# Kernel tuning notes

Hardware: AMD Instinct MI355X
Metric: run time of the kernel (lower is better)

## Reference

```python
import jax, jax.numpy as jnp
import numpy as np

N_NODES = 100000
N_EDGES = 1600000
N_IN = 512
N_H = 64


def setup_inputs() -> dict:
    key = jax.random.key(0)
    ks = jax.random.split(key, 9)
    x_1 = jax.random.normal(ks[0], (1, N_NODES, N_IN), dtype=jnp.float32)
    x_2 = jax.random.normal(ks[1], (1, N_NODES, N_IN), dtype=jnp.float32)
    edge_row = jax.random.randint(ks[2], (N_EDGES,), 0, N_NODES, dtype=jnp.int32)
    edge_col = jax.random.randint(ks[3], (N_EDGES,), 0, N_NODES, dtype=jnp.int32)
    edge_weight = jax.random.uniform(ks[4], (N_EDGES,), dtype=jnp.float32)
    # GCN fc: Linear(n_in, n_h, bias=False), xavier_uniform init
    lim_fc = float(np.sqrt(6.0 / (N_IN + N_H)))
    fc_weight = jax.random.uniform(ks[5], (N_H, N_IN), minval=-lim_fc, maxval=lim_fc, dtype=jnp.float32)
    gcn_bias = jnp.zeros((N_H,), dtype=jnp.float32)
    prelu_a = jnp.array(0.25, dtype=jnp.float32)  # nn.PReLU default single weight
    lim_lin = float(np.sqrt(1.0 / N_H))  # torch Linear default init bound
    lin_weight = jax.random.uniform(ks[6], (N_H, N_H), minval=-lim_lin, maxval=lim_lin, dtype=jnp.float32)
    lin_bias = jax.random.uniform(ks[7], (N_H,), minval=-lim_lin, maxval=lim_lin, dtype=jnp.float32)
    return {
        "x_1": x_1, "x_2": x_2,
        "edge_row": edge_row, "edge_col": edge_col, "edge_weight": edge_weight,
        "fc_weight": fc_weight, "gcn_bias": gcn_bias, "prelu_a": prelu_a,
        "lin_weight": lin_weight, "lin_bias": lin_bias,
    }


def reference(x_1, x_2, edge_row, edge_col, edge_weight,
              fc_weight, gcn_bias, prelu_a, lin_weight, lin_bias):
    def gcn(x):
        # fc: [1,N,F] @ W^T -> [N, H]
        h = jnp.einsum('bnf,hf->bnh', x, fc_weight)[0]
        # spmm: out[r] += w * h[c]  (COO adjacency)
        msgs = edge_weight[:, None] * h[edge_col]            # [E, H]
        agg = jax.ops.segment_sum(msgs, edge_row, num_segments=N_NODES)
        out = agg + gcn_bias
        return jnp.where(out >= 0, out, prelu_a * out)       # PReLU, shape [N, H]

    h_1 = gcn(x_1)
    h_2 = gcn(x_2)
    z_1 = (h_1 @ lin_weight.T + lin_bias).sum(axis=1)        # [N]
    z_2 = (h_2 @ lin_weight.T + lin_bias).sum(axis=1)        # [N]
    return jnp.concatenate([z_1, z_2], axis=0)               # [2N]
```

## Files before the change

kernel.cpp:

```cpp
#include <hip/hip_runtime.h>

#define F_IN 512
#define HDIM 64
#define RSHIFT 7
#define RWIDTH 128
#define MAXNB 1024
#define CHUNK 4096
#define BK 32

typedef _Float16 f16;
typedef _Float16 f16x2 __attribute__((ext_vector_type(2)));
typedef _Float16 f16x8 __attribute__((ext_vector_type(8)));
typedef float f32x4 __attribute__((ext_vector_type(4)));

#define GLOAD_LDS16(src, dst)                                                        \
    __builtin_amdgcn_global_load_lds((const __attribute__((address_space(1))) void*)(src), \
                                     (__attribute__((address_space(3))) void*)(dst), 16, 0, 0)

__global__ void prep_kernel(const float* __restrict__ linW,
                            const float* __restrict__ linB,
                            float* __restrict__ wsum) {
    int k = threadIdx.x;
    float s = 0.f;
    for (int j = 0; j < HDIM; ++j) s += linW[j * HDIM + k];
    wsum[k] = s;
    if (k == 0) {
        float b = 0.f;
        for (int j = 0; j < HDIM; ++j) b += linB[j];
        wsum[HDIM] = b;
    }
}

__global__ __launch_bounds__(256) void prep_w16_kernel(const float* __restrict__ W,
                                                       f16* __restrict__ wf) {
    int t = blockIdx.x * 256 + threadIdx.x;
    int s = t >> 8;
    int c = (t >> 6) & 3;
    int l = t & 63;
    int row = c * 16 + (l & 15);
    int kb = s * 32 + ((l >> 4) << 3);
#pragma unroll
    for (int j = 0; j < 8; ++j)
        wf[(size_t)t * 8 + j] = (f16)W[row * F_IN + kb + j];
}

__global__ void zero_int_kernel(int* __restrict__ p, int n) {
    int i = blockIdx.x * blockDim.x + threadIdx.x;
    if (i < n) p[i] = 0;
}

__global__ __launch_bounds__(256) void bhist_kernel(const int* __restrict__ row,
                                                    int* __restrict__ bh,
                                                    int n_edges, int NB) {
    __shared__ int lh[MAXNB];
    for (int i = threadIdx.x; i < NB; i += 256) lh[i] = 0;
    __syncthreads();
    for (int e = blockIdx.x * 256 + threadIdx.x; e < n_edges; e += gridDim.x * 256)
        atomicAdd(&lh[row[e] >> RSHIFT], 1);
    __syncthreads();
    for (int i = threadIdx.x; i < NB; i += 256)
        if (lh[i]) atomicAdd(&bh[i], lh[i]);
}

__global__ __launch_bounds__(1024) void bscan_kernel(const int* __restrict__ bh,
                                                     int* __restrict__ boff,
                                                     int* __restrict__ gcur,
                                                     int* __restrict__ ptr,
                                                     int NB, int n_nodes, int n_edges) {
    __shared__ int s[1024];
    const int t = threadIdx.x;
    int v = (t < NB) ? bh[t] : 0;
    s[t] = v;
    __syncthreads();
#pragma unroll
    for (int off = 1; off < 1024; off <<= 1) {
        int x = (t >= off) ? s[t - off] : 0;
        __syncthreads();
        s[t] += x;
        __syncthreads();
    }
    if (t < NB) {
        int o = s[t] - v;
        boff[t] = o;
        gcur[t] = o;
    }
    if (t == NB) boff[NB] = n_edges;
    if (t == 0) ptr[n_nodes] = n_edges;
}

__global__ __launch_bounds__(256) void part_kernel(const int* __restrict__ row,
                                                   const int* __restrict__ col,
                                                   const float* __restrict__ w,
                                                   int* __restrict__ gcur,
                                                   int2* __restrict__ etmp,
                                                   int n_edges, int NB) {
    __shared__ int2 stg[CHUNK];
    __shared__ unsigned short sbin[CHUNK];
    __shared__ int lh[MAXNB];
    __shared__ int lofs[MAXNB];
    __shared__ int psum[256];
    const int t = threadIdx.x;
    const int base = blockIdx.x * CHUNK;
    const int cnt = min(CHUNK, n_edges - base);

    for (int i = t; i < NB; i += 256) lh[i] = 0;
    __syncthreads();
    for (int i = t; i < cnt; i += 256)
        atomicAdd(&lh[row[base + i] >> RSHIFT], 1);
    __syncthreads();
    int loc[4];
    int s0 = 0;
#pragma unroll
    for (int j = 0; j < 4; ++j) {
        int b = t * 4 + j;
        int c = (b < NB) ? lh[b] : 0;
        loc[j] = s0;
        s0 += c;
    }
    psum[t] = s0;
    __syncthreads();
#pragma unroll
    for (int off = 1; off < 256; off <<= 1) {
        int x = (t >= off) ? psum[t - off] : 0;
        __syncthreads();
        psum[t] += x;
        __syncthreads();
    }
    int pbase = psum[t] - s0;
#pragma unroll
    for (int j = 0; j < 4; ++j) {
        int b = t * 4 + j;
        if (b < NB) lofs[b] = pbase + loc[j];
    }
    __syncthreads();
    for (int i = t; i < cnt; i += 256) {
        int r = row[base + i];
        int b = r >> RSHIFT;
        int p = atomicAdd(&lofs[b], 1);
        stg[p] = make_int2(__float_as_int(w[base + i]),
                           (col[base + i] << RSHIFT) | (r & (RWIDTH - 1)));
        sbin[p] = (unsigned short)b;
    }
    __syncthreads();
    for (int b = t; b < NB; b += 256) {
        int c = lh[b];
        if (c) {
            int lstart = lofs[b] - c;
            int gb = atomicAdd(&gcur[b], c);
            lh[b] = gb - lstart;
        }
    }
    __syncthreads();
    for (int p = t; p < cnt; p += 256) {
        int b = sbin[p];
        etmp[lh[b] + p] = stg[p];
    }
}

__global__ __launch_bounds__(256) void bsort_kernel(const int* __restrict__ boff,
                                                    const int2* __restrict__ etmp,
                                                    int2* __restrict__ ebin,
                                                    int* __restrict__ ptr,
                                                    int n_nodes) {
    __shared__ int nh[RWIDTH], lo[RWIDTH], lc[RWIDTH];
    const int b = blockIdx.x;
    const int t = threadIdx.x;
    const int e0 = boff[b], e1 = boff[b + 1];
    const int cnt = e1 - e0;
    if (t < RWIDTH) nh[t] = 0;
    __syncthreads();
    for (int i = t; i < cnt; i += 256)
        atomicAdd(&nh[etmp[e0 + i].y & (RWIDTH - 1)], 1);
    __syncthreads();
    if (t < RWIDTH) lo[t] = nh[t];
    __syncthreads();
    for (int off = 1; off < RWIDTH; off <<= 1) {
        int x = 0;
        if (t < RWIDTH && t >= off) x = lo[t - off];
        __syncthreads();
        if (t < RWIDTH) lo[t] += x;
        __syncthreads();
    }
    if (t < RWIDTH) {
        int ex = lo[t] - nh[t];
        lc[t] = ex;
        int node = b * RWIDTH + t;
        if (node < n_nodes) ptr[node] = e0 + ex;
    }
    __syncthreads();
    for (int i = t; i < cnt; i += 256) {
        int2 r = etmp[e0 + i];
        int p = atomicAdd(&lc[r.y & (RWIDTH - 1)], 1);
        ebin[e0 + p] = make_int2(r.x, r.y >> RSHIFT);
    }
}

__global__ __launch_bounds__(256, 4) void gemm_both_kernel(const float* __restrict__ X1,
                                                           const float* __restrict__ X2,
                                                           const f16* __restrict__ wf,
                                                           f16* __restrict__ H,
                                                           int n_nodes) {
    __shared__ float4 xs_v[2048];
    char* xs = (char*)xs_v;
    const int t = threadIdx.x;
    const int l = t & 63;
    const int w = t >> 6;
    const int m0 = blockIdx.x * 64;
    const f16x8* wfv = reinterpret_cast<const f16x8*>(wf);

    const int srow_off = l >> 3;
    const int sswz = (((l & 7) ^ (l >> 3)) << 4);

#define STAGE(c, buf)                                                                   \
    {                                                                                   \
        _Pragma("unroll")                                                               \
        for (int p = 0; p < 4; ++p) {                                                   \
            int row = ((p & 1) << 5) + (w << 3) + srow_off;                             \
            int gm = m0 + row;                                                          \
            if (gm >= n_nodes) gm = n_nodes - 1;                                        \
            const float* Xp = (p >> 1) ? X2 : X1;                                       \
            const char* src = (const char*)(Xp + (size_t)gm * F_IN + (c) * BK) + sswz;  \
            GLOAD_LDS16(src, xs + (buf) * 16384 + p * 4096 + w * 1024);                 \
        }                                                                               \
    }

    const int rl = w * 16 + (l & 15);
    const int g = l >> 4;
    const int swz = (rl & 7) << 4;

    f32x4 a00 = {}, a01 = {}, a02 = {}, a03 = {};
    f32x4 a10 = {}, a11 = {}, a12 = {}, a13 = {};

    STAGE(0, 0)
    __syncthreads();
    int buf = 0;
#pragma unroll 2
    for (int c = 0; c < 16; ++c) {
        if (c < 15) STAGE(c + 1, buf ^ 1)
        const f16x8* bp = wfv + (size_t)(c * 4) * 64 + l;
        f16x8 b0 = bp[0];
        f16x8 b1 = bp[64];
        f16x8 b2 = bp[128];
        f16x8 b3 = bp[192];
        const char* base = xs + buf * 16384 + rl * 128;
#pragma unroll
        for (int pass = 0; pass < 2; ++pass) {
            float4 xa = *reinterpret_cast<const float4*>(base + pass * 8192 + ((g * 32) ^ swz));
            float4 xb = *reinterpret_cast<const float4*>(base + pass * 8192 + ((g * 32 + 16) ^ swz));
            f16x8 a;
            a[0] = (f16)xa.x; a[1] = (f16)xa.y; a[2] = (f16)xa.z; a[3] = (f16)xa.w;
            a[4] = (f16)xb.x; a[5] = (f16)xb.y; a[6] = (f16)xb.z; a[7] = (f16)xb.w;
            if (pass == 0) {
                a00 = __builtin_amdgcn_mfma_f32_16x16x32_f16(a, b0, a00, 0, 0, 0);
                a01 = __builtin_amdgcn_mfma_f32_16x16x32_f16(a, b1, a01, 0, 0, 0);
                a02 = __builtin_amdgcn_mfma_f32_16x16x32_f16(a, b2, a02, 0, 0, 0);
                a03 = __builtin_amdgcn_mfma_f32_16x16x32_f16(a, b3, a03, 0, 0, 0);
            } else {
                a10 = __builtin_amdgcn_mfma_f32_16x16x32_f16(a, b0, a10, 0, 0, 0);
                a11 = __builtin_amdgcn_mfma_f32_16x16x32_f16(a, b1, a11, 0, 0, 0);
                a12 = __builtin_amdgcn_mfma_f32_16x16x32_f16(a, b2, a12, 0, 0, 0);
                a13 = __builtin_amdgcn_mfma_f32_16x16x32_f16(a, b3, a13, 0, 0, 0);
            }
        }
        __syncthreads();
        buf ^= 1;
    }
#undef STAGE

    {
        f16* tile = (f16*)xs;
        const int colj = l & 15;
        const int rbase = w * 16 + g * 4;
#pragma unroll
        for (int j = 0; j < 4; ++j) {
            f16* tp = tile + (rbase + j) * 128 + colj * 2;
            tp[0]  = (f16)a00[j];
            tp[1]  = (f16)a10[j];
            tp[32] = (f16)a01[j];
            tp[33] = (f16)a11[j];
            tp[64] = (f16)a02[j];
            tp[65] = (f16)a12[j];
            tp[96] = (f16)a03[j];
            tp[97] = (f16)a13[j];
        }
        __syncthreads();
        const int row = t >> 2;
        const int gm = m0 + row;
        if (gm < n_nodes) {
            const float4* sp = reinterpret_cast<const float4*>(xs + row * 256 + (t & 3) * 64);
            float4* dp = reinterpret_cast<float4*>((char*)H + (size_t)gm * 256 + (t & 3) * 64);
#pragma unroll
            for (int q = 0; q < 4; ++q) dp[q] = sp[q];
        }
    }
}

__global__ __launch_bounds__(256) void agg_both_kernel(const int* __restrict__ ptr,
                                                       const int2* __restrict__ ebin,
                                                       const f16* __restrict__ h,
                                                       const float* __restrict__ gbias,
                                                       const float* __restrict__ wsum,
                                                       const float* __restrict__ prelu_a,
                                                       float* __restrict__ z,
                                                       int n_nodes) {
    const int lane = threadIdx.x & 63;
    const int wv = threadIdx.x >> 6;
    const int n = blockIdx.x * 4 + wv;
    if (n >= n_nodes) return;
    const f16x2* hv = reinterpret_cast<const f16x2*>(h) + lane;
    const int p0 = __builtin_amdgcn_readfirstlane(ptr[n]);
    const int p1 = __builtin_amdgcn_readfirstlane(ptr[n + 1]);
    float acc1 = 0.f, acc2 = 0.f;
    int i = p0;
    for (; i + 3 < p1; i += 4) {
        int2 e0 = ebin[i];
        int2 e1 = ebin[i + 1];
        int2 e2 = ebin[i + 2];
        int2 e3 = ebin[i + 3];
        f16x2 h0 = hv[(size_t)e0.y * HDIM];
        f16x2 h1 = hv[(size_t)e1.y * HDIM];
        f16x2 h2 = hv[(size_t)e2.y * HDIM];
        f16x2 h3 = hv[(size_t)e3.y * HDIM];
        float w0 = __int_as_float(e0.x), w1 = __int_as_float(e1.x);
        float w2 = __int_as_float(e2.x), w3 = __int_as_float(e3.x);
        acc1 = fmaf(w0, (float)h0[0], acc1);
        acc2 = fmaf(w0, (float)h0[1], acc2);
        acc1 = fmaf(w1, (float)h1[0], acc1);
        acc2 = fmaf(w1, (float)h1[1], acc2);
        acc1 = fmaf(w2, (float)h2[0], acc1);
        acc2 = fmaf(w2, (float)h2[1], acc2);
        acc1 = fmaf(w3, (float)h3[0], acc1);
        acc2 = fmaf(w3, (float)h3[1], acc2);
    }
    for (; i < p1; ++i) {
        int2 e0 = ebin[i];
        f16x2 h0 = hv[(size_t)e0.y * HDIM];
        float w0 = __int_as_float(e0.x);
        acc1 = fmaf(w0, (float)h0[0], acc1);
        acc2 = fmaf(w0, (float)h0[1], acc2);
    }
    const float a = prelu_a[0];
    const float gb = gbias[lane];
    const float wl = wsum[lane];
    float v1 = acc1 + gb;
    float v2 = acc2 + gb;
    v1 = (v1 >= 0.f) ? v1 : a * v1;
    v2 = (v2 >= 0.f) ? v2 : a * v2;
    float q1 = v1 * wl;
    float q2 = v2 * wl;
#pragma unroll
    for (int m = 32; m >= 1; m >>= 1) {
        q1 += __shfl_xor(q1, m, 64);
        q2 += __shfl_xor(q2, m, 64);
    }
    if (lane == 0) {
        z[n] = q1 + wsum[HDIM];
        z[n + n_nodes] = q2 + wsum[HDIM];
    }
}

extern "C" void kernel_launch(void* const* d_in, const int* in_sizes, int n_in,
                              void* d_out, int out_size, void* d_ws, size_t ws_size,
                              hipStream_t stream) {
    const float* x1    = (const float*)d_in[0];
    const float* x2    = (const float*)d_in[1];
    const int*   erow  = (const int*)d_in[2];
    const int*   ecol  = (const int*)d_in[3];
    const float* ew    = (const float*)d_in[4];
    const float* fcw   = (const float*)d_in[5];
    const float* gbias = (const float*)d_in[6];
    const float* pa    = (const float*)d_in[7];
    const float* linw  = (const float*)d_in[8];
    const float* linb  = (const float*)d_in[9];
    float* out = (float*)d_out;

    const int n_nodes = in_sizes[0] / F_IN;
    const int n_edges = in_sizes[2];
    const int NB = (n_nodes + RWIDTH - 1) >> RSHIFT;

    f16*   h16  = (f16*)d_ws;
    f16*   wf   = h16 + (size_t)n_nodes * 2 * HDIM;
    int2*  etmp = (int2*)(wf + 64 * F_IN);
    int2*  ebin = etmp + n_edges;
    int*   bh   = (int*)(ebin + n_edges);
    int*   boff = bh + MAXNB;
    int*   gcur = boff + MAXNB + 1;
    int*   ptr  = gcur + MAXNB;
    float* wsum = (float*)(ptr + n_nodes + 1);

    prep_kernel<<<1, 64, 0, stream>>>(linw, linb, wsum);
    prep_w16_kernel<<<16, 256, 0, stream>>>(fcw, wf);

    zero_int_kernel<<<(NB + 255) / 256, 256, 0, stream>>>(bh, NB);
    bhist_kernel<<<256, 256, 0, stream>>>(erow, bh, n_edges, NB);
    bscan_kernel<<<1, 1024, 0, stream>>>(bh, boff, gcur, ptr, NB, n_nodes, n_edges);
    part_kernel<<<(n_edges + CHUNK - 1) / CHUNK, 256, 0, stream>>>(erow, ecol, ew, gcur,
                                                                   etmp, n_edges, NB);
    bsort_kernel<<<NB, 256, 0, stream>>>(boff, etmp, ebin, ptr, n_nodes);

    const int gemm_grid = (n_nodes + 63) / 64;
    const int fin_grid  = (n_nodes + 3) / 4;
    gemm_both_kernel<<<gemm_grid, 256, 0, stream>>>(x1, x2, wf, h16, n_nodes);
    agg_both_kernel<<<fin_grid, 256, 0, stream>>>(ptr, ebin, h16, gbias, wsum, pa,
                                                  out, n_nodes);
}
```

Before: 234.4 us.

## Load GEMM A operand directly from global into registers with software double buffering

The fused GCN projection GEMM no longer stages X tiles into LDS with global_load_lds and a double-buffered shared buffer with block barriers. Each lane now reads its fp32 X fragments straight from global memory into registers, using a two-stage register ping-pong for both X and the fp16 weight fragments, so the per-chunk __syncthreads disappear. LDS shrinks to just the output staging tile and the launch-bounds occupancy hint is removed. The trade-off is per-lane 32-byte strided global reads in place of coalesced LDS staging, plus higher register pressure that may reduce occupancy.

```diff
diff --git a/kernel.cpp b/kernel.cpp
--- a/kernel.cpp
+++ b/kernel.cpp
@@ -6,16 +6,11 @@
 #define RWIDTH 128
 #define MAXNB 1024
 #define CHUNK 4096
-#define BK 32
 
 typedef _Float16 f16;
 typedef _Float16 f16x2 __attribute__((ext_vector_type(2)));
 typedef _Float16 f16x8 __attribute__((ext_vector_type(8)));
 typedef float f32x4 __attribute__((ext_vector_type(4)));
-
-#define GLOAD_LDS16(src, dst)                                                        \
-    __builtin_amdgcn_global_load_lds((const __attribute__((address_space(1))) void*)(src), \
-                                     (__attribute__((address_space(3))) void*)(dst), 16, 0, 0)
 
 __global__ void prep_kernel(const float* __restrict__ linW,
                             const float* __restrict__ linB,
@@ -195,82 +190,83 @@
     }
 }
 
-__global__ __launch_bounds__(256, 4) void gemm_both_kernel(const float* __restrict__ X1,
-                                                           const float* __restrict__ X2,
-                                                           const f16* __restrict__ wf,
-                                                           f16* __restrict__ H,
-                                                           int n_nodes) {
-    __shared__ float4 xs_v[2048];
-    char* xs = (char*)xs_v;
+__global__ __launch_bounds__(256) void gemm_both_kernel(const float* __restrict__ X1,
+                                                        const float* __restrict__ X2,
+                                                        const f16* __restrict__ wf,
+                                                        f16* __restrict__ H,
+                                                        int n_nodes) {
+    __shared__ float4 tile_v[1024];
     const int t = threadIdx.x;
     const int l = t & 63;
     const int w = t >> 6;
     const int m0 = blockIdx.x * 64;
-    const f16x8* wfv = reinterpret_cast<const f16x8*>(wf);
-
-    const int srow_off = l >> 3;
-    const int sswz = (((l & 7) ^ (l >> 3)) << 4);
-
-#define STAGE(c, buf)                                                                   \
-    {                                                                                   \
-        _Pragma("unroll")                                                               \
-        for (int p = 0; p < 4; ++p) {                                                   \
-            int row = ((p & 1) << 5) + (w << 3) + srow_off;                             \
-            int gm = m0 + row;                                                          \
-            if (gm >= n_nodes) gm = n_nodes - 1;                                        \
-            const float* Xp = (p >> 1) ? X2 : X1;                                       \
-            const char* src = (const char*)(Xp + (size_t)gm * F_IN + (c) * BK) + sswz;  \
-            GLOAD_LDS16(src, xs + (buf) * 16384 + p * 4096 + w * 1024);                 \
-        }                                                                               \
-    }
-
-    const int rl = w * 16 + (l & 15);
+    int arow = m0 + w * 16 + (l & 15);
+    if (arow >= n_nodes) arow = n_nodes - 1;
     const int g = l >> 4;
-    const int swz = (rl & 7) << 4;
+    const float* xp1 = X1 + (size_t)arow * F_IN + (g << 3);
+    const float* xp2 = X2 + (size_t)arow * F_IN + (g << 3);
+    const f16x8* wfv = reinterpret_cast<const f16x8*>(wf) + l;
 
     f32x4 a00 = {}, a01 = {}, a02 = {}, a03 = {};
     f32x4 a10 = {}, a11 = {}, a12 = {}, a13 = {};
 
-    STAGE(0, 0)
-    __syncthreads();
-    int buf = 0;
-#pragma unroll 2
-    for (int c = 0; c < 16; ++c) {
-        if (c < 15) STAGE(c + 1, buf ^ 1)
-        const f16x8* bp = wfv + (size_t)(c * 4) * 64 + l;
-        f16x8 b0 = bp[0];
-        f16x8 b1 = bp[64];
-        f16x8 b2 = bp[128];
-        f16x8 b3 = bp[192];
-        const char* base = xs + buf * 16384 + rl * 128;
-#pragma unroll
-        for (int pass = 0; pass < 2; ++pass) {
-            float4 xa = *reinterpret_cast<const float4*>(base + pass * 8192 + ((g * 32) ^ swz));
-            float4 xb = *reinterpret_cast<const float4*>(base + pass * 8192 + ((g * 32 + 16) ^ swz));
-            f16x8 a;
-            a[0] = (f16)xa.x; a[1] = (f16)xa.y; a[2] = (f16)xa.z; a[3] = (f16)xa.w;
-            a[4] = (f16)xb.x; a[5] = (f16)xb.y; a[6] = (f16)xb.z; a[7] = (f16)xb.w;
-            if (pass == 0) {
-                a00 = __builtin_amdgcn_mfma_f32_16x16x32_f16(a, b0, a00, 0, 0, 0);
-                a01 = __builtin_amdgcn_mfma_f32_16x16x32_f16(a, b1, a01, 0, 0, 0);
-                a02 = __builtin_amdgcn_mfma_f32_16x16x32_f16(a, b2, a02, 0, 0, 0);
-                a03 = __builtin_amdgcn_mfma_f32_16x16x32_f16(a, b3, a03, 0, 0, 0);
-            } else {
-                a10 = __builtin_amdgcn_mfma_f32_16x16x32_f16(a, b0, a10, 0, 0, 0);
-                a11 = __builtin_amdgcn_mfma_f32_16x16x32_f16(a, b1, a11, 0, 0, 0);
-                a12 = __builtin_amdgcn_mfma_f32_16x16x32_f16(a, b2, a12, 0, 0, 0);
-                a13 = __builtin_amdgcn_mfma_f32_16x16x32_f16(a, b3, a13, 0, 0, 0);
-            }
+    float4 xa0A, xb0A, xa1A, xb1A; f16x8 B0A, B1A, B2A, B3A;
+    float4 xa0B, xb0B, xa1B, xb1B; f16x8 B0B, B1B, B2B, B3B;
+
+#define LD_X(d0a, d0b, d1a, d1b, c)                                   \
+    d0a = *reinterpret_cast<const float4*>(xp1 + (c) * 32);           \
+    d0b = *reinterpret_cast<const float4*>(xp1 + (c) * 32 + 4);       \
+    d1a = *reinterpret_cast<const float4*>(xp2 + (c) * 32);           \
+    d1b = *reinterpret_cast<const float4*>(xp2 + (c) * 32 + 4);
+
+#define LD_B(d0, d1, d2, d3, c)                                       \
+    {                                                                 \
+        const f16x8* bp = wfv + (size_t)(c) * 256;                    \
+        d0 = bp[0]; d1 = bp[64]; d2 = bp[128]; d3 = bp[192];          \
+    }
+
+#define COMP(xa0, xb0, xa1, xb1, b0, b1, b2, b3)                              \
+    {                                                                         \
+        f16x8 a;                                                              \
+        a[0] = (f16)xa0.x; a[1] = (f16)xa0.y; a[2] = (f16)xa0.z;              \
+        a[3] = (f16)xa0.w; a[4] = (f16)xb0.x; a[5] = (f16)xb0.y;              \
+        a[6] = (f16)xb0.z; a[7] = (f16)xb0.w;                                 \
+        a00 = __builtin_amdgcn_mfma_f32_16x16x32_f16(a, b0, a00, 0, 0, 0);    \
+        a01 = __builtin_amdgcn_mfma_f32_16x16x32_f16(a, b1, a01, 0, 0, 0);    \
+        a02 = __builtin_amdgcn_mfma_f32_16x16x32_f16(a, b2, a02, 0, 0, 0);    \
+        a03 = __builtin_amdgcn_mfma_f32_16x16x32_f16(a, b3, a03, 0, 0, 0);    \
+        a[0] = (f16)xa1.x; a[1] = (f16)xa1.y; a[2] = (f16)xa1.z;              \
+        a[3] = (f16)xa1.w; a[4] = (f16)xb1.x; a[5] = (f16)xb1.y;              \
+        a[6] = (f16)xb1.z; a[7] = (f16)xb1.w;                                 \
+        a10 = __builtin_amdgcn_mfma_f32_16x16x32_f16(a, b0, a10, 0, 0, 0);    \
+        a11 = __builtin_amdgcn_mfma_f32_16x16x32_f16(a, b1, a11, 0, 0, 0);    \
+        a12 = __builtin_amdgcn_mfma_f32_16x16x32_f16(a, b2, a12, 0, 0, 0);    \
+        a13 = __builtin_amdgcn_mfma_f32_16x16x32_f16(a, b3, a13, 0, 0, 0);    \
+    }
+
+    LD_X(xa0A, xb0A, xa1A, xb1A, 0)
+    LD_B(B0A, B1A, B2A, B3A, 0)
+#pragma unroll
+    for (int cc = 0; cc < 8; ++cc) {
+        const int c1 = 2 * cc + 1;
+        LD_X(xa0B, xb0B, xa1B, xb1B, c1)
+        LD_B(B0B, B1B, B2B, B3B, c1)
+        COMP(xa0A, xb0A, xa1A, xb1A, B0A, B1A, B2A, B3A)
+        if (cc < 7) {
+            LD_X(xa0A, xb0A, xa1A, xb1A, c1 + 1)
+            LD_B(B0A, B1A, B2A, B3A, c1 + 1)
         }
-        __syncthreads();
-        buf ^= 1;
-    }
-#undef STAGE
+        COMP(xa0B, xb0B, xa1B, xb1B, B0B, B1B, B2B, B3B)
+    }
+#undef LD_X
+#undef LD_B
+#undef COMP
 
     {
-        f16* tile = (f16*)xs;
+        f16* tile = (f16*)tile_v;
         const int colj = l & 15;
         const int rbase = w * 16 + g * 4;
+        __syncthreads();
 #pragma unroll
         for (int j = 0; j < 4; ++j) {
             f16* tp = tile + (rbase + j) * 128 + colj * 2;
@@ -287,7 +283,7 @@
         const int row = t >> 2;
         const int gm = m0 + row;
         if (gm < n_nodes) {
-            const float4* sp = reinterpret_cast<const float4*>(xs + row * 256 + (t & 3) * 64);
+            const float4* sp = reinterpret_cast<const float4*>((char*)tile + row * 256 + (t & 3) * 64);
             float4* dp = reinterpret_cast<float4*>((char*)H + (size_t)gm * 256 + (t & 3) * 64);
 #pragma unroll
             for (int q = 0; q < 4; ++q) dp[q] = sp[q];
```

Result: no change. 232.5 us (-0.8%).

## Process X1 and X2 sequentially in GEMM to halve LDS and raise occupancy

Applied to the files above, without the earlier changes.

The fused dual-input GEMM now runs two sequential passes, first X1 and then X2, each with a 16KB double-buffered LDS stage instead of a 32KB stage that held both inputs. The first pass's accumulators are packed to f16 pairs so only four f32x4 accumulators stay live, and launch bounds rise to 6 waves per SIMD. The LDS layout changes to a row-per-lane staging without the XOR swizzle, and the B-fragment loads are software-prefetched one step ahead. The aim is more resident blocks to hide global load latency. In exchange there are twice as many barriers and smaller load batches per sync, and the unswizzled layout risks bank conflicts.

```diff
diff --git a/kernel.cpp b/kernel.cpp
--- a/kernel.cpp
+++ b/kernel.cpp
@@ -6,7 +6,6 @@
 #define RWIDTH 128
 #define MAXNB 1024
 #define CHUNK 4096
-#define BK 32
 
 typedef _Float16 f16;
 typedef _Float16 f16x2 __attribute__((ext_vector_type(2)));
@@ -195,93 +194,111 @@
     }
 }
 
-__global__ __launch_bounds__(256, 4) void gemm_both_kernel(const float* __restrict__ X1,
+__global__ __launch_bounds__(256, 6) void gemm_both_kernel(const float* __restrict__ X1,
                                                            const float* __restrict__ X2,
                                                            const f16* __restrict__ wf,
                                                            f16* __restrict__ H,
                                                            int n_nodes) {
-    __shared__ float4 xs_v[2048];
-    char* xs = (char*)xs_v;
+    __shared__ float4 lds4[1024];
+    char* xs = (char*)lds4;
     const int t = threadIdx.x;
     const int l = t & 63;
     const int w = t >> 6;
     const int m0 = blockIdx.x * 64;
-    const f16x8* wfv = reinterpret_cast<const f16x8*>(wf);
-
-    const int srow_off = l >> 3;
-    const int sswz = (((l & 7) ^ (l >> 3)) << 4);
-
-#define STAGE(c, buf)                                                                   \
-    {                                                                                   \
-        _Pragma("unroll")                                                               \
-        for (int p = 0; p < 4; ++p) {                                                   \
-            int row = ((p & 1) << 5) + (w << 3) + srow_off;                             \
-            int gm = m0 + row;                                                          \
-            if (gm >= n_nodes) gm = n_nodes - 1;                                        \
-            const float* Xp = (p >> 1) ? X2 : X1;                                       \
-            const char* src = (const char*)(Xp + (size_t)gm * F_IN + (c) * BK) + sswz;  \
-            GLOAD_LDS16(src, xs + (buf) * 16384 + p * 4096 + w * 1024);                 \
-        }                                                                               \
-    }
-
-    const int rl = w * 16 + (l & 15);
+
+    int srow = m0 + l;
+    if (srow >= n_nodes) srow = n_nodes - 1;
+    const char* sb1 = (const char*)(X1 + (size_t)srow * F_IN) + w * 32;
+    const char* sb2 = (const char*)(X2 + (size_t)srow * F_IN) + w * 32;
+
     const int g = l >> 4;
-    const int swz = (rl & 7) << 4;
-
-    f32x4 a00 = {}, a01 = {}, a02 = {}, a03 = {};
-    f32x4 a10 = {}, a11 = {}, a12 = {}, a13 = {};
-
-    STAGE(0, 0)
-    __syncthreads();
-    int buf = 0;
-#pragma unroll 2
+    const int rl16 = (w * 16 + (l & 15)) * 16;
+    const int a0 = g * 2048 + rl16;
+
+    const f16x8* wfv = reinterpret_cast<const f16x8*>(wf) + l;
+    const int colj = l & 15;
+    const int rbase = w * 16 + g * 4;
+
+    f32x4 ac0 = {}, ac1 = {}, ac2 = {}, ac3 = {};
+    f16x8 B0, B1, B2, B3;
+    f16x2 p0a, p0b, p1a, p1b, p2a, p2b, p3a, p3b;
+
+#define STAGE(base, c, buf)                                                  \
+    GLOAD_LDS16((base) + (c) * 128,      xs + (buf) * 8192 + w * 2048);      \
+    GLOAD_LDS16((base) + (c) * 128 + 16, xs + (buf) * 8192 + w * 2048 + 1024);
+
+#define LOADB(c)                                                             \
+    { const f16x8* bp = wfv + (size_t)(c) * 256;                             \
+      B0 = bp[0]; B1 = bp[64]; B2 = bp[128]; B3 = bp[192]; }
+
+#define COMPUTE(buf)                                                              \
+    {                                                                             \
+        float4 xa = *reinterpret_cast<const float4*>(xs + (buf) * 8192 + a0);     \
+        float4 xb = *reinterpret_cast<const float4*>(xs + (buf) * 8192 + a0 + 1024); \
+        f16x8 a;                                                                  \
+        a[0] = (f16)xa.x; a[1] = (f16)xa.y; a[2] = (f16)xa.z; a[3] = (f16)xa.w;   \
+        a[4] = (f16)xb.x; a[5] = (f16)xb.y; a[6] = (f16)xb.z; a[7] = (f16)xb.w;   \
+        ac0 = __builtin_amdgcn_mfma_f32_16x16x32_f16(a, B0, ac0, 0, 0, 0);        \
+        ac1 = __builtin_amdgcn_mfma_f32_16x16x32_f16(a, B1, ac1, 0, 0, 0);        \
+        ac2 = __builtin_amdgcn_mfma_f32_16x16x32_f16(a, B2, ac2, 0, 0, 0);        \
+        ac3 = __builtin_amdgcn_mfma_f32_16x16x32_f16(a, B3, ac3, 0, 0, 0);        \
+    }
+
+    STAGE(sb1, 0, 0)
+    LOADB(0)
+    __syncthreads();
+#pragma unroll
     for (int c = 0; c < 16; ++c) {
-        if (c < 15) STAGE(c + 1, buf ^ 1)
-        const f16x8* bp = wfv + (size_t)(c * 4) * 64 + l;
-        f16x8 b0 = bp[0];
-        f16x8 b1 = bp[64];
-        f16x8 b2 = bp[128];
-        f16x8 b3 = bp[192];
-        const char* base = xs + buf * 16384 + rl * 128;
-#pragma unroll
-        for (int pass = 0; pass < 2; ++pass) {
-            float4 xa = *reinterpret_cast<const float4*>(base + pass * 8192 + ((g * 32) ^ swz));
-            float4 xb = *reinterpret_cast<const float4*>(base + pass * 8192 + ((g * 32 + 16) ^ swz));
-            f16x8 a;
-            a[0] = (f16)xa.x; a[1] = (f16)xa.y; a[2] = (f16)xa.z; a[3] = (f16)xa.w;
-            a[4] = (f16)xb.x; a[5] = (f16)xb.y; a[6] = (f16)xb.z; a[7] = (f16)xb.w;
-            if (pass == 0) {
-                a00 = __builtin_amdgcn_mfma_f32_16x16x32_f16(a, b0, a00, 0, 0, 0);
-                a01 = __builtin_amdgcn_mfma_f32_16x16x32_f16(a, b1, a01, 0, 0, 0);
-                a02 = __builtin_amdgcn_mfma_f32_16x16x32_f16(a, b2, a02, 0, 0, 0);
-                a03 = __builtin_amdgcn_mfma_f32_16x16x32_f16(a, b3, a03, 0, 0, 0);
-            } else {
-                a10 = __builtin_amdgcn_mfma_f32_16x16x32_f16(a, b0, a10, 0, 0, 0);
-                a11 = __builtin_amdgcn_mfma_f32_16x16x32_f16(a, b1, a11, 0, 0, 0);
-                a12 = __builtin_amdgcn_mfma_f32_16x16x32_f16(a, b2, a12, 0, 0, 0);
-                a13 = __builtin_amdgcn_mfma_f32_16x16x32_f16(a, b3, a13, 0, 0, 0);
-            }
-        }
-        __syncthreads();
-        buf ^= 1;
+        COMPUTE(c & 1)
+        if (c < 15) {
+            STAGE(sb1, c + 1, (c + 1) & 1)
+            LOADB(c + 1)
+        }
+        __syncthreads();
+    }
+    p0a = f16x2{(f16)ac0[0], (f16)ac0[1]}; p0b = f16x2{(f16)ac0[2], (f16)ac0[3]};
+    p1a = f16x2{(f16)ac1[0], (f16)ac1[1]}; p1b = f16x2{(f16)ac1[2], (f16)ac1[3]};
+    p2a = f16x2{(f16)ac2[0], (f16)ac2[1]}; p2b = f16x2{(f16)ac2[2], (f16)ac2[3]};
+    p3a = f16x2{(f16)ac3[0], (f16)ac3[1]}; p3b = f16x2{(f16)ac3[2], (f16)ac3[3]};
+    ac0 = f32x4{}; ac1 = f32x4{}; ac2 = f32x4{}; ac3 = f32x4{};
+
+    STAGE(sb2, 0, 0)
+    LOADB(0)
+    __syncthreads();
+#pragma unroll
+    for (int c = 0; c < 16; ++c) {
+        COMPUTE(c & 1)
+        if (c < 15) {
+            STAGE(sb2, c + 1, (c + 1) & 1)
+            LOADB(c + 1)
+        }
+        __syncthreads();
     }
 #undef STAGE
+#undef LOADB
+#undef COMPUTE
 
     {
         f16* tile = (f16*)xs;
-        const int colj = l & 15;
-        const int rbase = w * 16 + g * 4;
-#pragma unroll
-        for (int j = 0; j < 4; ++j) {
-            f16* tp = tile + (rbase + j) * 128 + colj * 2;
-            tp[0]  = (f16)a00[j];
-            tp[1]  = (f16)a10[j];
-            tp[32] = (f16)a01[j];
-            tp[33] = (f16)a11[j];
-            tp[64] = (f16)a02[j];
-            tp[65] = (f16)a12[j];
-            tp[96] = (f16)a03[j];
-            tp[97] = (f16)a13[j];
+        {
+            f16* tp = tile + (rbase + 0) * 128 + colj * 2;
+            tp[0] = p0a[0]; tp[32] = p1a[0]; tp[64] = p2a[0]; tp[96] = p3a[0];
+            tp[1] = (f16)ac0[0]; tp[33] = (f16)ac1[0]; tp[65] = (f16)ac2[0]; tp[97] = (f16)ac3[0];
+        }
+        {
+            f16* tp = tile + (rbase + 1) * 128 + colj * 2;
+            tp[0] = p0a[1]; tp[32] = p1a[1]; tp[64] = p2a[1]; tp[96] = p3a[1];
+            tp[1] = (f16)ac0[1]; tp[33] = (f16)ac1[1]; tp[65] = (f16)ac2[1]; tp[97] = (f16)ac3[1];
+        }
+        {
+            f16* tp = tile + (rbase + 2) * 128 + colj * 2;
+            tp[0] = p0b[0]; tp[32] = p1b[0]; tp[64] = p2b[0]; tp[96] = p3b[0];
+            tp[1] = (f16)ac0[2]; tp[33] = (f16)ac1[2]; tp[65] = (f16)ac2[2]; tp[97] = (f16)ac3[2];
+        }
+        {
+            f16* tp = tile + (rbase + 3) * 128 + colj * 2;
+            tp[0] = p0b[1]; tp[32] = p1b[1]; tp[64] = p2b[1]; tp[96] = p3b[1];
+            tp[1] = (f16)ac0[3]; tp[33] = (f16)ac1[3]; tp[65] = (f16)ac2[3]; tp[97] = (f16)ac3[3];
         }
         __syncthreads();
         const int row = t >> 2;
```

New measurement: 271.3 us. 15.7% more time.
